# Kernel tuning notes

Measured on AMD Instinct MI355X. Metric: run time of the kernel, lower is better.

## Reference

```python
import jax, jax.numpy as jnp
import numpy as np

TEMPERATURE = 0.07
MASK_VALUE = -10000.0
EPS = 1e-12  # matches F.normalize eps


def setup_inputs() -> dict:
    key = jax.random.key(0)
    k1, k2 = jax.random.split(key)
    B, D = 8192, 512
    embeddings = jax.random.normal(k1, (B, D), dtype=jnp.float32)
    positive_mask = jax.random.randint(k2, (B, B), 0, 2).astype(bool)
    return {"embeddings": embeddings, "positive_mask": positive_mask}


def reference(embeddings, positive_mask):
    B = embeddings.shape[0]
    # L2 normalize rows (F.normalize with eps clamp)
    norm = jnp.maximum(jnp.linalg.norm(embeddings, axis=1, keepdims=True), EPS)
    e = embeddings / norm
    sim = jnp.matmul(e, e.T) / TEMPERATURE  # (B, B)
    eye = jnp.eye(B, dtype=bool)
    sim = jnp.where(eye, MASK_VALUE, sim)
    pos = positive_mask & ~eye
    counts = pos.sum(axis=1)  # (B,)
    pos_sum = jnp.sum(jnp.where(pos, sim, 0.0), axis=1)  # (B,)
    lse = jax.nn.logsumexp(sim, axis=1)  # (B,)
    pos_mean = pos_sum / jnp.maximum(counts, 1).astype(sim.dtype)
    # rows with positives: -mean(pos) + lse; rows without: just lse
    row_loss = jnp.where(counts > 0, lse - pos_mean, lse)
    return jnp.mean(row_loss)
```

## Files before the change

### kernel.cpp

```cpp
#include <hip/hip_runtime.h>
#include <hip/hip_bf16.h>

#define BN_ 8192
#define DK_ 512
#define TEMP_INV 14.2857142857142857f
#define LOG2E_ 1.44269504088896f
#define MAXOFF 15.0f

typedef __bf16 bf16x8 __attribute__((ext_vector_type(8)));
typedef float f32x4 __attribute__((ext_vector_type(4)));

__device__ inline unsigned short f2bf(float f) {
    unsigned u = __float_as_uint(f);
    return (unsigned short)((u + 0x7FFFu + ((u >> 16) & 1u)) >> 16);
}

__global__ __launch_bounds__(256) void norm_kernel(const float* __restrict__ emb,
                                                   unsigned short* __restrict__ ebf,
                                                   float* __restrict__ zero3,
                                                   float* __restrict__ out) {
    const int t = threadIdx.x;
    if (blockIdx.x < 96) zero3[blockIdx.x * 256 + t] = 0.0f;
    else if (blockIdx.x == 96 && t == 0) out[0] = 0.0f;

    const int row  = blockIdx.x * 4 + (t >> 6);
    const int lane = t & 63;
    const float4* src = reinterpret_cast<const float4*>(emb + (size_t)row * DK_);
    float4 v0 = src[lane];
    float4 v1 = src[lane + 64];
    float ss = v0.x*v0.x + v0.y*v0.y + v0.z*v0.z + v0.w*v0.w
             + v1.x*v1.x + v1.y*v1.y + v1.z*v1.z + v1.w*v1.w;
#pragma unroll
    for (int off = 1; off < 64; off <<= 1) ss += __shfl_xor(ss, off, 64);
    const float scale = 1.0f / fmaxf(sqrtf(ss), 1e-12f);
    uint2 o0, o1;
    o0.x = (unsigned)f2bf(v0.x * scale) | ((unsigned)f2bf(v0.y * scale) << 16);
    o0.y = (unsigned)f2bf(v0.z * scale) | ((unsigned)f2bf(v0.w * scale) << 16);
    o1.x = (unsigned)f2bf(v1.x * scale) | ((unsigned)f2bf(v1.y * scale) << 16);
    o1.y = (unsigned)f2bf(v1.z * scale) | ((unsigned)f2bf(v1.w * scale) << 16);
    uint2* dst = reinterpret_cast<uint2*>(ebf + (size_t)row * DK_);
    dst[lane]      = o0;
    dst[lane + 64] = o1;
}

__global__ __launch_bounds__(256, 4) void infonce_main(
    const unsigned short* __restrict__ ebf,
    const int* __restrict__ mask,
    float* __restrict__ se, float* __restrict__ ps, float* __restrict__ ct) {

    __shared__ unsigned short As[128 * 64];
    __shared__ unsigned short Bs[128 * 64];
    __shared__ unsigned char  pmB[128 * 16];
    __shared__ float red2[2][128];

    const int t    = threadIdx.x;
    const int lane = t & 63;
    const int wid  = t >> 6;
    const int wr   = wid >> 1;
    const int wc   = wid & 1;
    const int rb   = blockIdx.x;
    const int cb   = blockIdx.y;

    if (t < 128) { red2[0][t] = 0.f; red2[1][t] = 0.f; }

    f32x4 acc[4][4] = {};

    const int sr  = t >> 3;
    const int scs = (((t & 7) ^ (sr & 7)) * 8);
    const size_t arow0 = (size_t)(rb * 128 + sr) * DK_ + scs;
    const size_t brow0 = (size_t)(cb * 128 + sr) * DK_ + scs;

    const int mr = t >> 4;
    const int mc = t & 15;
    const int* mbase = mask + (size_t)(rb * 128 + mr) * BN_ + cb * 128 + mc * 8;

    const int r16 = lane & 15;
    const int g4  = lane >> 4;
    const int r7  = r16 & 7;

#define STAGE(kt)                                                                          \
    {                                                                                      \
        const int k0_ = (kt) * 64;                                                         \
        _Pragma("unroll")                                                                  \
        for (int s = 0; s < 4; ++s) {                                                      \
            __builtin_amdgcn_global_load_lds(                                              \
                (const __attribute__((address_space(1))) void*)(ebf + arow0 + (size_t)s * 32 * DK_ + k0_), \
                (__attribute__((address_space(3))) void*)(As + s * 2048 + t * 8),          \
                16, 0, 0);                                                                 \
        }                                                                                  \
        _Pragma("unroll")                                                                  \
        for (int s = 0; s < 4; ++s) {                                                      \
            __builtin_amdgcn_global_load_lds(                                              \
                (const __attribute__((address_space(1))) void*)(ebf + brow0 + (size_t)s * 32 * DK_ + k0_), \
                (__attribute__((address_space(3))) void*)(Bs + s * 2048 + t * 8),          \
                16, 0, 0);                                                                 \
        }                                                                                  \
    }

    int4 m0[2], m1[2];

    { const int4* p = reinterpret_cast<const int4*>(mbase); m0[0] = p[0]; m1[0] = p[1]; }
    asm volatile("" ::: "memory");

#pragma unroll
    for (int kt = 0; kt < 8; ++kt) {
        STAGE(kt);
        asm volatile("" ::: "memory");
        if (kt < 7) {
            const int4* p = reinterpret_cast<const int4*>(mbase + (size_t)(kt + 1) * 16 * BN_);
            m0[(kt + 1) & 1] = p[0];
            m1[(kt + 1) & 1] = p[1];
        }
        asm volatile("" ::: "memory");
        if (kt < 7) { asm volatile("s_waitcnt vmcnt(2)" ::: "memory"); }
        else        { asm volatile("s_waitcnt vmcnt(0)" ::: "memory"); }
        __builtin_amdgcn_s_barrier();
        __builtin_amdgcn_sched_barrier(0);

        {
            const int4 a = m0[kt & 1], b = m1[kt & 1];
            unsigned by = (unsigned)(a.x != 0)        | ((unsigned)(a.y != 0) << 1)
                        | ((unsigned)(a.z != 0) << 2) | ((unsigned)(a.w != 0) << 3)
                        | ((unsigned)(b.x != 0) << 4) | ((unsigned)(b.y != 0) << 5)
                        | ((unsigned)(b.z != 0) << 6) | ((unsigned)(b.w != 0) << 7);
            pmB[(kt * 16 + mr) * 16 + mc] = (unsigned char)by;
        }

#pragma unroll
        for (int ks = 0; ks < 2; ++ks) {
            bf16x8 af[4], bfr[4];
            const int koff = (((ks * 4 + g4) ^ r7) * 8);
#pragma unroll
            for (int fm = 0; fm < 4; ++fm)
                af[fm] = *reinterpret_cast<const bf16x8*>(As + (wr * 64 + fm * 16 + r16) * 64 + koff);
#pragma unroll
            for (int fn = 0; fn < 4; ++fn)
                bfr[fn] = *reinterpret_cast<const bf16x8*>(Bs + (wc * 64 + fn * 16 + r16) * 64 + koff);
#pragma unroll
            for (int fm = 0; fm < 4; ++fm)
#pragma unroll
                for (int fn = 0; fn < 4; ++fn)
                    acc[fm][fn] = __builtin_amdgcn_mfma_f32_16x16x32_bf16(bfr[fn], af[fm], acc[fm][fn], 0, 0, 0);
        }
        __builtin_amdgcn_sched_barrier(0);
        __builtin_amdgcn_s_barrier();
        __builtin_amdgcn_sched_barrier(0);
    }
#undef STAGE
    __syncthreads();

    const float C1 = TEMP_INV * LOG2E_;
    const float C2 = -MAXOFF * LOG2E_;
    const bool  db  = (rb == cb);
    const int   gq4 = (lane >> 4) * 4;

#pragma unroll
    for (int fm = 0; fm < 4; ++fm) {
        const int li = wr * 64 + fm * 16 + (lane & 15);
        const uint4 rv = *reinterpret_cast<const uint4*>(pmB + li * 16);
        const unsigned w0 = wc ? rv.z : rv.x;
        const unsigned w1 = wc ? rv.w : rv.y;
        float lsep = 0.f, posp = 0.f;
#pragma unroll
        for (int fn = 0; fn < 4; ++fn) {
            const unsigned wsel = (fn < 2) ? w0 : w1;
#pragma unroll
            for (int rg = 0; rg < 4; ++rg) {
                const float a = acc[fm][fn][rg];
                const bool dg = db && (wr == wc) && (fm == fn) && ((lane & 15) == gq4 + rg);
                const float ex = dg ? 0.0f : exp2f(fmaf(a, C1, C2));
                lsep += ex;
                const bool p = (((wsel >> ((fn & 1) * 16 + gq4 + rg)) & 1u) != 0u) && !dg;
                posp += p ? a : 0.0f;
            }
        }
        lsep += __shfl_xor(lsep, 16, 64); lsep += __shfl_xor(lsep, 32, 64);
        posp += __shfl_xor(posp, 16, 64); posp += __shfl_xor(posp, 32, 64);
        if ((lane >> 4) == 0) {
            atomicAdd(&red2[0][li], lsep);
            atomicAdd(&red2[1][li], posp * TEMP_INV);
        }
    }
    __syncthreads();
    if (t < 128) {
        const uint4 rv = *reinterpret_cast<const uint4*>(pmB + t * 16);
        float cnt = (float)(__popc(rv.x) + __popc(rv.y) + __popc(rv.z) + __popc(rv.w));
        if (db) {
            const unsigned wsel = (t < 64) ? ((t < 32) ? rv.x : rv.y)
                                           : ((t < 96) ? rv.z : rv.w);
            cnt -= (float)((wsel >> (t & 31)) & 1u);
        }
        const int i = rb * 128 + t;
        atomicAdd(&se[i], red2[0][t]);
        atomicAdd(&ps[i], red2[1][t]);
        atomicAdd(&ct[i], cnt);
    }
}

__global__ __launch_bounds__(256) void finalize_kernel(const float* __restrict__ se,
                                                       const float* __restrict__ ps,
                                                       const float* __restrict__ ct,
                                                       float* __restrict__ out) {
    __shared__ float red[256];
    const int t = threadIdx.x;
    const int i = blockIdx.x * 256 + t;
    const float lse = logf(se[i]) + MAXOFF;
    red[t] = lse - ps[i] / fmaxf(ct[i], 1.0f);
    __syncthreads();
    for (int s = 128; s > 0; s >>= 1) {
        if (t < s) red[t] += red[t + s];
        __syncthreads();
    }
    if (t == 0) atomicAdd(out, red[0] * (1.0f / (float)BN_));
}

extern "C" void kernel_launch(void* const* d_in, const int* in_sizes, int n_in,
                              void* d_out, int out_size, void* d_ws, size_t ws_size,
                              hipStream_t stream) {
    const float* emb  = (const float*)d_in[0];
    const int*   mask = (const int*)d_in[1];
    float* out = (float*)d_out;

    char* ws = (char*)d_ws;
    unsigned short* ebf = (unsigned short*)ws;
    float* se = (float*)(ws + (size_t)8 * 1024 * 1024);
    float* ps = se + BN_;
    float* ct = ps + BN_;

    norm_kernel<<<BN_ / 4, 256, 0, stream>>>(emb, ebf, se, out);
    infonce_main<<<dim3(64, 64), 256, 0, stream>>>(ebf, mask, se, ps, ct);
    finalize_kernel<<<BN_ / 256, 256, 0, stream>>>(se, ps, ct, out);
}
```

Before: 111.2 us.

## Enlarge GEMM tile to 256x256 with double-buffered LDS and interleaved loads

The main kernel moves from 128x128 tiles with 4 waves to 256x256 tiles with 8 waves, each wave computing a 128x64 sub-tile. LDS is double-buffered, and the next K-slice loads plus mask reads are spread across four sub-steps with fine-grained vmcnt waits, so memory traffic overlaps MFMA work. MFMA sections run at raised priority via s_setprio. The larger tile cuts global re-reads of the embeddings, but it uses far more LDS and registers (acc[8][4]), lowering occupancy. It also leaves 1024 blocks, which may fill the 256 CUs less evenly.

```diff
diff --git a/kernel.cpp b/kernel.cpp
--- a/kernel.cpp
+++ b/kernel.cpp
@@ -43,131 +43,167 @@
     dst[lane + 64] = o1;
 }
 
-__global__ __launch_bounds__(256, 4) void infonce_main(
+__global__ __launch_bounds__(512, 2) void infonce_main(
     const unsigned short* __restrict__ ebf,
     const int* __restrict__ mask,
     float* __restrict__ se, float* __restrict__ ps, float* __restrict__ ct) {
 
-    __shared__ unsigned short As[128 * 64];
-    __shared__ unsigned short Bs[128 * 64];
-    __shared__ unsigned char  pmB[128 * 16];
-    __shared__ float red2[2][128];
+    __shared__ unsigned short As[2][256 * 64];
+    __shared__ unsigned short Bs[2][256 * 64];
+    __shared__ unsigned char  pmB[256 * 32];
+    __shared__ float red2[2][256];
 
     const int t    = threadIdx.x;
     const int lane = t & 63;
     const int wid  = t >> 6;
-    const int wr   = wid >> 1;
-    const int wc   = wid & 1;
+    const int wr   = wid >> 2;
+    const int wc   = wid & 3;
     const int rb   = blockIdx.x;
     const int cb   = blockIdx.y;
 
-    if (t < 128) { red2[0][t] = 0.f; red2[1][t] = 0.f; }
-
-    f32x4 acc[4][4] = {};
+    if (t < 256) { red2[0][t] = 0.f; red2[1][t] = 0.f; }
+
+    f32x4 acc[8][4] = {};
 
     const int sr  = t >> 3;
     const int scs = (((t & 7) ^ (sr & 7)) * 8);
-    const size_t arow0 = (size_t)(rb * 128 + sr) * DK_ + scs;
-    const size_t brow0 = (size_t)(cb * 128 + sr) * DK_ + scs;
-
-    const int mr = t >> 4;
-    const int mc = t & 15;
-    const int* mbase = mask + (size_t)(rb * 128 + mr) * BN_ + cb * 128 + mc * 8;
+    const size_t aoff = (size_t)(rb * 256 + sr) * DK_ + scs;
+    const size_t boff = (size_t)(cb * 256 + sr) * DK_ + scs;
+
+    const int mrow = t >> 1;
+    const int mhalf = t & 1;
+    const int* mbase = mask + (size_t)(rb * 256 + mrow) * BN_ + cb * 256 + mhalf * 16;
 
     const int r16 = lane & 15;
     const int g4  = lane >> 4;
     const int r7  = r16 & 7;
-
-#define STAGE(kt)                                                                          \
-    {                                                                                      \
-        const int k0_ = (kt) * 64;                                                         \
-        _Pragma("unroll")                                                                  \
-        for (int s = 0; s < 4; ++s) {                                                      \
-            __builtin_amdgcn_global_load_lds(                                              \
-                (const __attribute__((address_space(1))) void*)(ebf + arow0 + (size_t)s * 32 * DK_ + k0_), \
-                (__attribute__((address_space(3))) void*)(As + s * 2048 + t * 8),          \
-                16, 0, 0);                                                                 \
-        }                                                                                  \
-        _Pragma("unroll")                                                                  \
-        for (int s = 0; s < 4; ++s) {                                                      \
-            __builtin_amdgcn_global_load_lds(                                              \
-                (const __attribute__((address_space(1))) void*)(ebf + brow0 + (size_t)s * 32 * DK_ + k0_), \
-                (__attribute__((address_space(3))) void*)(Bs + s * 2048 + t * 8),          \
-                16, 0, 0);                                                                 \
-        }                                                                                  \
-    }
-
-    int4 m0[2], m1[2];
-
-    { const int4* p = reinterpret_cast<const int4*>(mbase); m0[0] = p[0]; m1[0] = p[1]; }
-    asm volatile("" ::: "memory");
+    const int gq4 = g4 * 4;
+
+#define SLD(dst, soff) __builtin_amdgcn_global_load_lds(                                   \
+        (const __attribute__((address_space(1))) void*)(ebf + (soff)),                     \
+        (__attribute__((address_space(3))) void*)((dst) + t * 8), 16, 0, 0)
+#define FENCE asm volatile("" ::: "memory")
+
+    int4 mreg[2][4];
+
+    SLD(&Bs[0][0],        boff);
+    SLD(&Bs[0][64 * 64],  boff + (size_t)64 * DK_);
+    FENCE;
+    mreg[0][0] = *reinterpret_cast<const int4*>(mbase + 0);
+    FENCE;
+    SLD(&Bs[0][128 * 64], boff + (size_t)128 * DK_);
+    SLD(&Bs[0][192 * 64], boff + (size_t)192 * DK_);
+    FENCE;
+    mreg[0][1] = *reinterpret_cast<const int4*>(mbase + 4);
+    FENCE;
+    SLD(&As[0][0],        aoff);
+    SLD(&As[0][128 * 64], aoff + (size_t)128 * DK_);
+    FENCE;
+    mreg[0][2] = *reinterpret_cast<const int4*>(mbase + 8);
+    FENCE;
+    SLD(&As[0][64 * 64],  aoff + (size_t)64 * DK_);
+    SLD(&As[0][192 * 64], aoff + (size_t)192 * DK_);
+    FENCE;
+    mreg[0][3] = *reinterpret_cast<const int4*>(mbase + 12);
+    FENCE;
 
 #pragma unroll
     for (int kt = 0; kt < 8; ++kt) {
-        STAGE(kt);
-        asm volatile("" ::: "memory");
-        if (kt < 7) {
-            const int4* p = reinterpret_cast<const int4*>(mbase + (size_t)(kt + 1) * 16 * BN_);
-            m0[(kt + 1) & 1] = p[0];
-            m1[(kt + 1) & 1] = p[1];
-        }
-        asm volatile("" ::: "memory");
-        if (kt < 7) { asm volatile("s_waitcnt vmcnt(2)" ::: "memory"); }
-        else        { asm volatile("s_waitcnt vmcnt(0)" ::: "memory"); }
-        __builtin_amdgcn_s_barrier();
-        __builtin_amdgcn_sched_barrier(0);
-
-        {
-            const int4 a = m0[kt & 1], b = m1[kt & 1];
-            unsigned by = (unsigned)(a.x != 0)        | ((unsigned)(a.y != 0) << 1)
-                        | ((unsigned)(a.z != 0) << 2) | ((unsigned)(a.w != 0) << 3)
-                        | ((unsigned)(b.x != 0) << 4) | ((unsigned)(b.y != 0) << 5)
-                        | ((unsigned)(b.z != 0) << 6) | ((unsigned)(b.w != 0) << 7);
-            pmB[(kt * 16 + mr) * 16 + mc] = (unsigned char)by;
-        }
-
-#pragma unroll
-        for (int ks = 0; ks < 2; ++ks) {
-            bf16x8 af[4], bfr[4];
+        const int b = kt & 1;
+#pragma unroll
+        for (int q = 0; q < 4; ++q) {
+            if (kt < 7) {
+                const int nb = b ^ 1;
+                const size_t k1 = (size_t)(kt + 1) * 64;
+                if (q == 0) {
+                    SLD(&Bs[nb][0],        boff + k1);
+                    SLD(&Bs[nb][64 * 64],  boff + (size_t)64 * DK_ + k1);
+                } else if (q == 1) {
+                    SLD(&Bs[nb][128 * 64], boff + (size_t)128 * DK_ + k1);
+                    SLD(&Bs[nb][192 * 64], boff + (size_t)192 * DK_ + k1);
+                } else if (q == 2) {
+                    SLD(&As[nb][0],        aoff + k1);
+                    SLD(&As[nb][128 * 64], aoff + (size_t)128 * DK_ + k1);
+                } else {
+                    SLD(&As[nb][64 * 64],  aoff + (size_t)64 * DK_ + k1);
+                    SLD(&As[nb][192 * 64], aoff + (size_t)192 * DK_ + k1);
+                }
+                FENCE;
+                mreg[(kt + 1) & 1][q] =
+                    *reinterpret_cast<const int4*>(mbase + (size_t)(kt + 1) * 32 + q * 4);
+                FENCE;
+            }
+            if (kt < 7) {
+                if (q == 0 || q == 1) { asm volatile("s_waitcnt vmcnt(7)" ::: "memory"); }
+                else if (q == 2)      { asm volatile("s_waitcnt vmcnt(9)" ::: "memory"); }
+            } else {
+                if (q == 0)      { asm volatile("s_waitcnt vmcnt(4)" ::: "memory"); }
+                else if (q == 1) { asm volatile("s_waitcnt vmcnt(1)" ::: "memory"); }
+                else if (q == 2) { asm volatile("s_waitcnt vmcnt(0)" ::: "memory"); }
+            }
+            __builtin_amdgcn_s_barrier();
+            __builtin_amdgcn_sched_barrier(0);
+
+            if (q == 2) {
+                unsigned bits = 0u;
+#pragma unroll
+                for (int j = 0; j < 4; ++j) {
+                    const int4 v = mreg[b][j];
+                    bits |= ((unsigned)(v.x != 0) << (j * 4))
+                          | ((unsigned)(v.y != 0) << (j * 4 + 1))
+                          | ((unsigned)(v.z != 0) << (j * 4 + 2))
+                          | ((unsigned)(v.w != 0) << (j * 4 + 3));
+                }
+                *reinterpret_cast<unsigned short*>(pmB + mrow * 32 + kt * 4 + mhalf * 2) =
+                    (unsigned short)bits;
+            }
+
+            const int fmh  = q & 1;
+            const int ks   = q >> 1;
             const int koff = (((ks * 4 + g4) ^ r7) * 8);
-#pragma unroll
-            for (int fm = 0; fm < 4; ++fm)
-                af[fm] = *reinterpret_cast<const bf16x8*>(As + (wr * 64 + fm * 16 + r16) * 64 + koff);
-#pragma unroll
-            for (int fn = 0; fn < 4; ++fn)
-                bfr[fn] = *reinterpret_cast<const bf16x8*>(Bs + (wc * 64 + fn * 16 + r16) * 64 + koff);
-#pragma unroll
-            for (int fm = 0; fm < 4; ++fm)
-#pragma unroll
-                for (int fn = 0; fn < 4; ++fn)
-                    acc[fm][fn] = __builtin_amdgcn_mfma_f32_16x16x32_bf16(bfr[fn], af[fm], acc[fm][fn], 0, 0, 0);
-        }
-        __builtin_amdgcn_sched_barrier(0);
-        __builtin_amdgcn_s_barrier();
-        __builtin_amdgcn_sched_barrier(0);
-    }
-#undef STAGE
+            bf16x8 af[4], bfv[4];
+#pragma unroll
+            for (int i = 0; i < 4; ++i)
+                af[i] = *reinterpret_cast<const bf16x8*>(
+                    &As[b][(wr * 128 + (fmh * 4 + i) * 16 + r16) * 64 + koff]);
+#pragma unroll
+            for (int i = 0; i < 4; ++i)
+                bfv[i] = *reinterpret_cast<const bf16x8*>(
+                    &Bs[b][(wc * 64 + i * 16 + r16) * 64 + koff]);
+            __builtin_amdgcn_s_setprio(1);
+#pragma unroll
+            for (int i = 0; i < 4; ++i)
+#pragma unroll
+                for (int j = 0; j < 4; ++j)
+                    acc[fmh * 4 + i][j] = __builtin_amdgcn_mfma_f32_16x16x32_bf16(
+                        bfv[j], af[i], acc[fmh * 4 + i][j], 0, 0, 0);
+            __builtin_amdgcn_s_setprio(0);
+            __builtin_amdgcn_sched_barrier(0);
+            __builtin_amdgcn_s_barrier();
+            __builtin_amdgcn_sched_barrier(0);
+        }
+    }
+#undef SLD
+#undef FENCE
     __syncthreads();
 
     const float C1 = TEMP_INV * LOG2E_;
     const float C2 = -MAXOFF * LOG2E_;
-    const bool  db  = (rb == cb);
-    const int   gq4 = (lane >> 4) * 4;
-
-#pragma unroll
-    for (int fm = 0; fm < 4; ++fm) {
-        const int li = wr * 64 + fm * 16 + (lane & 15);
-        const uint4 rv = *reinterpret_cast<const uint4*>(pmB + li * 16);
-        const unsigned w0 = wc ? rv.z : rv.x;
-        const unsigned w1 = wc ? rv.w : rv.y;
+    const bool  db = (rb == cb);
+
+#pragma unroll
+    for (int fm = 0; fm < 8; ++fm) {
+        const int li = wr * 128 + fm * 16 + r16;
+        const uint2 w = *reinterpret_cast<const uint2*>(pmB + li * 32 + wc * 8);
         float lsep = 0.f, posp = 0.f;
 #pragma unroll
         for (int fn = 0; fn < 4; ++fn) {
-            const unsigned wsel = (fn < 2) ? w0 : w1;
+            const unsigned wsel = (fn < 2) ? w.x : w.y;
 #pragma unroll
             for (int rg = 0; rg < 4; ++rg) {
+                const int jl = wc * 64 + fn * 16 + gq4 + rg;
                 const float a = acc[fm][fn][rg];
-                const bool dg = db && (wr == wc) && (fm == fn) && ((lane & 15) == gq4 + rg);
+                const bool dg = db && (jl == li);
                 const float ex = dg ? 0.0f : exp2f(fmaf(a, C1, C2));
                 lsep += ex;
                 const bool p = (((wsel >> ((fn & 1) * 16 + gq4 + rg)) & 1u) != 0u) && !dg;
@@ -176,21 +212,22 @@
         }
         lsep += __shfl_xor(lsep, 16, 64); lsep += __shfl_xor(lsep, 32, 64);
         posp += __shfl_xor(posp, 16, 64); posp += __shfl_xor(posp, 32, 64);
-        if ((lane >> 4) == 0) {
+        if (g4 == 0) {
             atomicAdd(&red2[0][li], lsep);
             atomicAdd(&red2[1][li], posp * TEMP_INV);
         }
     }
     __syncthreads();
-    if (t < 128) {
-        const uint4 rv = *reinterpret_cast<const uint4*>(pmB + t * 16);
-        float cnt = (float)(__popc(rv.x) + __popc(rv.y) + __popc(rv.z) + __popc(rv.w));
+    if (t < 256) {
+        const uint4 u0 = *reinterpret_cast<const uint4*>(pmB + t * 32);
+        const uint4 u1 = *reinterpret_cast<const uint4*>(pmB + t * 32 + 16);
+        float cnt = (float)(__popc(u0.x) + __popc(u0.y) + __popc(u0.z) + __popc(u0.w)
+                          + __popc(u1.x) + __popc(u1.y) + __popc(u1.z) + __popc(u1.w));
         if (db) {
-            const unsigned wsel = (t < 64) ? ((t < 32) ? rv.x : rv.y)
-                                           : ((t < 96) ? rv.z : rv.w);
-            cnt -= (float)((wsel >> (t & 31)) & 1u);
-        }
-        const int i = rb * 128 + t;
+            const unsigned wb = pmB[t * 32 + (t >> 3)];
+            cnt -= (float)((wb >> (t & 7)) & 1u);
+        }
+        const int i = rb * 256 + t;
         atomicAdd(&se[i], red2[0][t]);
         atomicAdd(&ps[i], red2[1][t]);
         atomicAdd(&ct[i], cnt);
@@ -228,6 +265,6 @@
     float* ct = ps + BN_;
 
     norm_kernel<<<BN_ / 4, 256, 0, stream>>>(emb, ebf, se, out);
-    infonce_main<<<dim3(64, 64), 256, 0, stream>>>(ebf, mask, se, ps, ct);
+    infonce_main<<<dim3(32, 32), 512, 0, stream>>>(ebf, mask, se, ps, ct);
     finalize_kernel<<<BN_ / 256, 256, 0, stream>>>(se, ps, ct, out);
 }
```

Result: slower. 143.6 us (+29.2%).
